# Kernel optimization log

Measured on AMD Instinct MI355X. Metric: run time of the kernel, lower is better.

The kernel has to match this reference:

```python
import jax, jax.numpy as jnp
import numpy as np

# BlendParams defaults (pytorch3d)
SIGMA = 1e-4
GAMMA = 1e-4
ZNEAR = 1.0
ZFAR = 100.0
EPS = 1e-10

N, H, W, K, C = 4, 256, 256, 8, 16
V, F = 100000, 200000


def setup_inputs() -> dict:
    key = jax.random.key(0)
    ks = jax.random.split(key, 7)
    return {
        "dists": jax.random.normal(ks[0], (N, H, W, K), dtype=jnp.float32),
        "zbuf": jax.random.uniform(ks[1], (N, H, W, K), dtype=jnp.float32),
        "bary_coords": jax.random.uniform(ks[2], (N, H, W, K, 3), dtype=jnp.float32),
        "verts_features": jax.random.normal(ks[3], (V, C), dtype=jnp.float32),
        "background": jax.random.uniform(ks[4], (C,), dtype=jnp.float32),
        "pix_to_face": jax.random.randint(ks[5], (N, H, W, K), 0, F),
        "faces": jax.random.randint(ks[6], (F, 3), 0, V),
    }


def reference(dists, zbuf, bary_coords, verts_features, background, pix_to_face, faces):
    mask = (pix_to_face >= 0)
    maskf = mask.astype(dists.dtype)
    safe_idx = jnp.where(mask, pix_to_face, 0)

    # --- sample_textures (TexturesVertex): barycentric gather ---
    # faces[safe_idx]: (N,H,W,K,3) vertex ids -> (N,H,W,K,3,C) features
    face_vert_feats = verts_features[faces[safe_idx]]
    texels = jnp.einsum("nhwkv,nhwkvc->nhwkc", bary_coords, face_vert_feats)

    # --- softmax_blend ---
    prob_map = jax.nn.sigmoid(-dists / SIGMA) * maskf                 # (N,H,W,K)
    z_inv = (ZFAR - zbuf) / (ZFAR - ZNEAR) * maskf                    # (N,H,W,K)
    z_inv_max = jnp.clip(jnp.max(z_inv, axis=-1, keepdims=True), EPS)  # (N,H,W,1)
    weights_num = prob_map * jnp.exp((z_inv - z_inv_max) / GAMMA)      # (N,H,W,K)
    delta = jnp.clip(jnp.exp((EPS - z_inv_max) / GAMMA), EPS)          # (N,H,W,1)
    denom = jnp.sum(weights_num, axis=-1, keepdims=True) + delta       # (N,H,W,1)

    weighted_colors = jnp.einsum("nhwk,nhwkc->nhwc", weights_num, texels)
    pixel_colors = (weighted_colors + delta * background) / denom      # (N,H,W,C)
    return pixel_colors
```

## Files before the change

kernel.cpp:

```cpp
#include <hip/hip_runtime.h>


constexpr int CC = 16;

typedef float floatx2 __attribute__((ext_vector_type(2)));
typedef float floatx4 __attribute__((ext_vector_type(4)));
typedef int   intx2   __attribute__((ext_vector_type(2)));

template <int CTRL>
__device__ __forceinline__ float dpp_movf(float x) {
    return __int_as_float(
        __builtin_amdgcn_mov_dpp(__float_as_int(x), CTRL, 0xF, 0xF, true));
}
#define DPP_XOR1 0xB1
#define DPP_XOR2 0x4E

#define GATHER_SLOT(F, TT, W)                                                \
    {                                                                        \
        int v0 = faces[(size_t)(F) * 3 + 0];                                 \
        int v1 = faces[(size_t)(F) * 3 + 1];                                 \
        int v2 = faces[(size_t)(F) * 3 + 2];                                 \
        const float* bp = bary + (size_t)(TT) * 3;                           \
        float b0 = bp[0] * (W), b1 = bp[1] * (W), b2 = bp[2] * (W);          \
        const float4* t0 = (const float4*)(vfeat + (size_t)v0 * CC);         \
        const float4* t1 = (const float4*)(vfeat + (size_t)v1 * CC);         \
        const float4* t2 = (const float4*)(vfeat + (size_t)v2 * CC);         \
        float4 a0, a1, a2;                                                   \
        a0 = t0[0]; a1 = t1[0]; a2 = t2[0];                                  \
        x0  += b0 * a0.x + b1 * a1.x + b2 * a2.x;                            \
        x1  += b0 * a0.y + b1 * a1.y + b2 * a2.y;                            \
        x2  += b0 * a0.z + b1 * a1.z + b2 * a2.z;                            \
        x3  += b0 * a0.w + b1 * a1.w + b2 * a2.w;                            \
        a0 = t0[1]; a1 = t1[1]; a2 = t2[1];                                  \
        x4  += b0 * a0.x + b1 * a1.x + b2 * a2.x;                            \
        x5  += b0 * a0.y + b1 * a1.y + b2 * a2.y;                            \
        x6  += b0 * a0.z + b1 * a1.z + b2 * a2.z;                            \
        x7  += b0 * a0.w + b1 * a1.w + b2 * a2.w;                            \
        a0 = t0[2]; a1 = t1[2]; a2 = t2[2];                                  \
        x8  += b0 * a0.x + b1 * a1.x + b2 * a2.x;                            \
        x9  += b0 * a0.y + b1 * a1.y + b2 * a2.y;                            \
        x10 += b0 * a0.z + b1 * a1.z + b2 * a2.z;                            \
        x11 += b0 * a0.w + b1 * a1.w + b2 * a2.w;                            \
        a0 = t0[3]; a1 = t1[3]; a2 = t2[3];                                  \
        x12 += b0 * a0.x + b1 * a1.x + b2 * a2.x;                            \
        x13 += b0 * a0.y + b1 * a1.y + b2 * a2.y;                            \
        x14 += b0 * a0.z + b1 * a1.z + b2 * a2.z;                            \
        x15 += b0 * a0.w + b1 * a1.w + b2 * a2.w;                            \
    }

__global__ __launch_bounds__(256) void feature_shader(
    const float* __restrict__ dists,
    const float* __restrict__ zbuf,
    const float* __restrict__ bary,
    const float* __restrict__ vfeat,
    const float* __restrict__ bg,
    const int*   __restrict__ p2f,
    const int*   __restrict__ faces,
    float* __restrict__ out,
    int n)
{
    const float INV_SIGMA = 1e4f;
    const float INV_GAMMA = 1e4f;
    const float EPS       = 1e-10f;
    const float ZFAR      = 100.f;
    const float INV_SPAN  = 1.f / 99.f;

    int u = blockIdx.x * blockDim.x + threadIdx.x;
    if (u >= (n >> 1)) return;
    int t = u << 1;
    int q = threadIdx.x & 3;

    floatx2 z2 = __builtin_nontemporal_load((const floatx2*)zbuf  + u);
    floatx2 d2 = __builtin_nontemporal_load((const floatx2*)dists + u);
    intx2   f2 = __builtin_nontemporal_load((const intx2*)  p2f   + u);
    int fa = f2.x, fb = f2.y;

    float zinv0 = (fa >= 0) ? (ZFAR - z2.x) * INV_SPAN : 0.f;
    float zinv1 = (fb >= 0) ? (ZFAR - z2.y) * INV_SPAN : 0.f;

    float m = fmaxf(zinv0, zinv1);
    m = fmaxf(m, dpp_movf<DPP_XOR1>(m));
    m = fmaxf(m, dpp_movf<DPP_XOR2>(m));
    m = fmaxf(m, EPS);

    float delta = fmaxf(__expf((EPS - m) * INV_GAMMA), EPS);
    float prob0 = (fa >= 0) ? 1.f / (1.f + __expf(d2.x * INV_SIGMA)) : 0.f;
    float prob1 = (fb >= 0) ? 1.f / (1.f + __expf(d2.y * INV_SIGMA)) : 0.f;
    float w0 = prob0 * __expf((zinv0 - m) * INV_GAMMA);
    float w1 = prob1 * __expf((zinv1 - m) * INV_GAMMA);

    float denom = w0 + w1;
    denom += dpp_movf<DPP_XOR1>(denom);
    denom += dpp_movf<DPP_XOR2>(denom);
    denom += delta;
    float thr = denom * 1e-7f;

    float x0 = 0.f, x1 = 0.f, x2 = 0.f, x3 = 0.f;
    float x4 = 0.f, x5 = 0.f, x6 = 0.f, x7 = 0.f;
    float x8 = 0.f, x9 = 0.f, x10 = 0.f, x11 = 0.f;
    float x12 = 0.f, x13 = 0.f, x14 = 0.f, x15 = 0.f;

    if (w0 > thr) GATHER_SLOT(fa, t,     w0);
    if (w1 > thr) GATHER_SLOT(fb, t + 1, w1);

    bool lo1 = (q & 1) == 0;
    float s, r;
    float e0, e1, e2, e3, e4, e5, e6, e7;
    s = lo1 ? x4  : x0;  r = dpp_movf<DPP_XOR1>(s);  e0 = (lo1 ? x0  : x4 ) + r;
    s = lo1 ? x5  : x1;  r = dpp_movf<DPP_XOR1>(s);  e1 = (lo1 ? x1  : x5 ) + r;
    s = lo1 ? x6  : x2;  r = dpp_movf<DPP_XOR1>(s);  e2 = (lo1 ? x2  : x6 ) + r;
    s = lo1 ? x7  : x3;  r = dpp_movf<DPP_XOR1>(s);  e3 = (lo1 ? x3  : x7 ) + r;
    s = lo1 ? x12 : x8;  r = dpp_movf<DPP_XOR1>(s);  e4 = (lo1 ? x8  : x12) + r;
    s = lo1 ? x13 : x9;  r = dpp_movf<DPP_XOR1>(s);  e5 = (lo1 ? x9  : x13) + r;
    s = lo1 ? x14 : x10; r = dpp_movf<DPP_XOR1>(s);  e6 = (lo1 ? x10 : x14) + r;
    s = lo1 ? x15 : x11; r = dpp_movf<DPP_XOR1>(s);  e7 = (lo1 ? x11 : x15) + r;

    bool lo2 = (q & 2) == 0;
    float g0, g1, g2, g3;
    s = lo2 ? e4 : e0;  r = dpp_movf<DPP_XOR2>(s);  g0 = (lo2 ? e0 : e4) + r;
    s = lo2 ? e5 : e1;  r = dpp_movf<DPP_XOR2>(s);  g1 = (lo2 ? e1 : e5) + r;
    s = lo2 ? e6 : e2;  r = dpp_movf<DPP_XOR2>(s);  g2 = (lo2 ? e2 : e6) + r;
    s = lo2 ? e7 : e3;  r = dpp_movf<DPP_XOR2>(s);  g3 = (lo2 ? e3 : e7) + r;

    float4 bgv = ((const float4*)bg)[q];
    float inv_den = 1.f / denom;
    floatx4 o;
    o.x = (g0 + delta * bgv.x) * inv_den;
    o.y = (g1 + delta * bgv.y) * inv_den;
    o.z = (g2 + delta * bgv.z) * inv_den;
    o.w = (g3 + delta * bgv.w) * inv_den;
    __builtin_nontemporal_store(o, (floatx4*)out + u);
}

extern "C" void kernel_launch(void* const* d_in, const int* in_sizes, int n_in,
                              void* d_out, int out_size, void* d_ws, size_t ws_size,
                              hipStream_t stream) {
    const float* dists = (const float*)d_in[0];
    const float* zbuf  = (const float*)d_in[1];
    const float* bary  = (const float*)d_in[2];
    const float* vfeat = (const float*)d_in[3];
    const float* bg    = (const float*)d_in[4];
    const int*   p2f   = (const int*)d_in[5];
    const int*   faces = (const int*)d_in[6];
    float* out = (float*)d_out;

    int n = in_sizes[0];
    int pairs = n >> 1;
    int block = 256;
    int grid = (pairs + block - 1) / block;

    hipLaunchKernelGGL(feature_shader, dim3(grid), dim3(block), 0, stream,
                       dists, zbuf, bary, vfeat, bg, p2f, faces, out, n);
}
```

Before: 118.8 us.

## Distribute face gathers across the lane quad by channel slice instead of by slot

```diff
diff --git a/kernel.cpp b/kernel.cpp
--- a/kernel.cpp
+++ b/kernel.cpp
@@ -8,44 +8,34 @@
 typedef int   intx2   __attribute__((ext_vector_type(2)));
 
 template <int CTRL>
+__device__ __forceinline__ int dpp_movi(int x) {
+    return __builtin_amdgcn_mov_dpp(x, CTRL, 0xF, 0xF, true);
+}
+template <int CTRL>
 __device__ __forceinline__ float dpp_movf(float x) {
-    return __int_as_float(
-        __builtin_amdgcn_mov_dpp(__float_as_int(x), CTRL, 0xF, 0xF, true));
+    return __int_as_float(dpp_movi<CTRL>(__float_as_int(x)));
 }
 #define DPP_XOR1 0xB1
 #define DPP_XOR2 0x4E
 
-#define GATHER_SLOT(F, TT, W)                                                \
+#define SLOT(OO, RR)                                                         \
     {                                                                        \
-        int v0 = faces[(size_t)(F) * 3 + 0];                                 \
-        int v1 = faces[(size_t)(F) * 3 + 1];                                 \
-        int v2 = faces[(size_t)(F) * 3 + 2];                                 \
-        const float* bp = bary + (size_t)(TT) * 3;                           \
-        float b0 = bp[0] * (W), b1 = bp[1] * (W), b2 = bp[2] * (W);          \
-        const float4* t0 = (const float4*)(vfeat + (size_t)v0 * CC);         \
-        const float4* t1 = (const float4*)(vfeat + (size_t)v1 * CC);         \
-        const float4* t2 = (const float4*)(vfeat + (size_t)v2 * CC);         \
-        float4 a0, a1, a2;                                                   \
-        a0 = t0[0]; a1 = t1[0]; a2 = t2[0];                                  \
-        x0  += b0 * a0.x + b1 * a1.x + b2 * a2.x;                            \
-        x1  += b0 * a0.y + b1 * a1.y + b2 * a2.y;                            \
-        x2  += b0 * a0.z + b1 * a1.z + b2 * a2.z;                            \
-        x3  += b0 * a0.w + b1 * a1.w + b2 * a2.w;                            \
-        a0 = t0[1]; a1 = t1[1]; a2 = t2[1];                                  \
-        x4  += b0 * a0.x + b1 * a1.x + b2 * a2.x;                            \
-        x5  += b0 * a0.y + b1 * a1.y + b2 * a2.y;                            \
-        x6  += b0 * a0.z + b1 * a1.z + b2 * a2.z;                            \
-        x7  += b0 * a0.w + b1 * a1.w + b2 * a2.w;                            \
-        a0 = t0[2]; a1 = t1[2]; a2 = t2[2];                                  \
-        x8  += b0 * a0.x + b1 * a1.x + b2 * a2.x;                            \
-        x9  += b0 * a0.y + b1 * a1.y + b2 * a2.y;                            \
-        x10 += b0 * a0.z + b1 * a1.z + b2 * a2.z;                            \
-        x11 += b0 * a0.w + b1 * a1.w + b2 * a2.w;                            \
-        a0 = t0[3]; a1 = t1[3]; a2 = t2[3];                                  \
-        x12 += b0 * a0.x + b1 * a1.x + b2 * a2.x;                            \
-        x13 += b0 * a0.y + b1 * a1.y + b2 * a2.y;                            \
-        x14 += b0 * a0.z + b1 * a1.z + b2 * a2.z;                            \
-        x15 += b0 * a0.w + b1 * a1.w + b2 * a2.w;                            \
+        float ws = dpp_movf<(OO) * 0x55>((RR) ? w1 : w0);                    \
+        if (ws > thr) {                 \
+            int fs = dpp_movi<(OO) * 0x55>((RR) ? fb : fa);                  \
+            int v0 = faces[(size_t)fs * 3 + 0];       \
+            int v1 = faces[(size_t)fs * 3 + 1];                              \
+            int v2 = faces[(size_t)fs * 3 + 2];                              \
+            const float* bp = bary + (base8 + (OO) * 2 + (RR)) * 3;          \
+            float c0 = bp[0] * ws, c1 = bp[1] * ws, c2 = bp[2] * ws;         \
+            float4 A0 = vf4[(size_t)v0 * 4 + q];   \
+            float4 A1 = vf4[(size_t)v1 * 4 + q];                             \
+            float4 A2 = vf4[(size_t)v2 * 4 + q];                             \
+            ax += c0 * A0.x + c1 * A1.x + c2 * A2.x;                         \
+            ay += c0 * A0.y + c1 * A1.y + c2 * A2.y;                         \
+            az += c0 * A0.z + c1 * A1.z + c2 * A2.z;                         \
+            aw += c0 * A0.w + c1 * A1.w + c2 * A2.w;                         \
+        }                                                                    \
     }
 
 __global__ __launch_bounds__(256) void feature_shader(
@@ -67,8 +57,8 @@
 
     int u = blockIdx.x * blockDim.x + threadIdx.x;
     if (u >= (n >> 1)) return;
-    int t = u << 1;
     int q = threadIdx.x & 3;
+    size_t base8 = (size_t)(u >> 2) * 8;
 
     floatx2 z2 = __builtin_nontemporal_load((const floatx2*)zbuf  + u);
     floatx2 d2 = __builtin_nontemporal_load((const floatx2*)dists + u);
@@ -95,40 +85,22 @@
     denom += delta;
     float thr = denom * 1e-7f;
 
-    float x0 = 0.f, x1 = 0.f, x2 = 0.f, x3 = 0.f;
-    float x4 = 0.f, x5 = 0.f, x6 = 0.f, x7 = 0.f;
-    float x8 = 0.f, x9 = 0.f, x10 = 0.f, x11 = 0.f;
-    float x12 = 0.f, x13 = 0.f, x14 = 0.f, x15 = 0.f;
+    float ax = 0.f, ay = 0.f, az = 0.f, aw = 0.f;
 
-    if (w0 > thr) GATHER_SLOT(fa, t,     w0);
-    if (w1 > thr) GATHER_SLOT(fb, t + 1, w1);
+    const float4* vf4 = (const float4*)vfeat;
 
-    bool lo1 = (q & 1) == 0;
-    float s, r;
-    float e0, e1, e2, e3, e4, e5, e6, e7;
-    s = lo1 ? x4  : x0;  r = dpp_movf<DPP_XOR1>(s);  e0 = (lo1 ? x0  : x4 ) + r;
-    s = lo1 ? x5  : x1;  r = dpp_movf<DPP_XOR1>(s);  e1 = (lo1 ? x1  : x5 ) + r;
-    s = lo1 ? x6  : x2;  r = dpp_movf<DPP_XOR1>(s);  e2 = (lo1 ? x2  : x6 ) + r;
-    s = lo1 ? x7  : x3;  r = dpp_movf<DPP_XOR1>(s);  e3 = (lo1 ? x3  : x7 ) + r;
-    s = lo1 ? x12 : x8;  r = dpp_movf<DPP_XOR1>(s);  e4 = (lo1 ? x8  : x12) + r;
-    s = lo1 ? x13 : x9;  r = dpp_movf<DPP_XOR1>(s);  e5 = (lo1 ? x9  : x13) + r;
-    s = lo1 ? x14 : x10; r = dpp_movf<DPP_XOR1>(s);  e6 = (lo1 ? x10 : x14) + r;
-    s = lo1 ? x15 : x11; r = dpp_movf<DPP_XOR1>(s);  e7 = (lo1 ? x11 : x15) + r;
-
-    bool lo2 = (q & 2) == 0;
-    float g0, g1, g2, g3;
-    s = lo2 ? e4 : e0;  r = dpp_movf<DPP_XOR2>(s);  g0 = (lo2 ? e0 : e4) + r;
-    s = lo2 ? e5 : e1;  r = dpp_movf<DPP_XOR2>(s);  g1 = (lo2 ? e1 : e5) + r;
-    s = lo2 ? e6 : e2;  r = dpp_movf<DPP_XOR2>(s);  g2 = (lo2 ? e2 : e6) + r;
-    s = lo2 ? e7 : e3;  r = dpp_movf<DPP_XOR2>(s);  g3 = (lo2 ? e3 : e7) + r;
+    SLOT(0, 0) SLOT(0, 1)
+    SLOT(1, 0) SLOT(1, 1)
+    SLOT(2, 0) SLOT(2, 1)
+    SLOT(3, 0) SLOT(3, 1)
 
     float4 bgv = ((const float4*)bg)[q];
     float inv_den = 1.f / denom;
     floatx4 o;
-    o.x = (g0 + delta * bgv.x) * inv_den;
-    o.y = (g1 + delta * bgv.y) * inv_den;
-    o.z = (g2 + delta * bgv.z) * inv_den;
-    o.w = (g3 + delta * bgv.w) * inv_den;
+    o.x = (ax + delta * bgv.x) * inv_den;
+    o.y = (ay + delta * bgv.y) * inv_den;
+    o.z = (az + delta * bgv.z) * inv_den;
+    o.w = (aw + delta * bgv.w) * inv_den;
     __builtin_nontemporal_store(o, (floatx4*)out + u);
 }
 
```

Result: slower. 121.2 us (+2.0%).
